# Kernel optimization log

Measured on AMD Instinct MI355X. Metric: run time of the kernel, lower is better.

## Reference

```python
import jax, jax.numpy as jnp
import numpy as np

N, D, K = 8192, 2048, 10000
EPS = 1e-12
COMMITMENT_COST = 0.25


def _l2_normalize(v, axis):
    # matches torch F.normalize(p=2): v / max(||v||, eps)
    n = jnp.linalg.norm(v, axis=axis, keepdims=True)
    return v / jnp.maximum(n, EPS)


def setup_inputs() -> dict:
    key = jax.random.key(0)
    kx, kw = jax.random.split(key)
    x = jax.random.normal(kx, (N, D), dtype=jnp.float32)
    # nn.Embedding weight initialized uniform(0, 3) per the module
    weight = jax.random.uniform(kw, (K, D), dtype=jnp.float32, minval=0.0, maxval=3.0)
    return {"x": x, "weight": weight}


def reference(x, weight):
    # --- get_code_indices ---
    xn = _l2_normalize(x, axis=1)          # [N, D]
    wn = _l2_normalize(weight, axis=1)     # [K, D]
    # ||xn||^2 + ||wn||^2 - 2 xn . wn  -> [N, K]
    distances = (
        jnp.sum(xn * xn, axis=1, keepdims=True)
        + jnp.sum(wn * wn, axis=1)
        - 2.0 * jnp.matmul(xn, wn.T)
    )
    encoding_indices = jnp.argmin(distances, axis=1)  # [N]
    # --- quantize (gathers the UN-normalized codebook, as in the module) ---
    quantized = weight[encoding_indices]              # [N, D]
    # --- training losses ---
    q_latent_loss = jnp.mean((quantized - jax.lax.stop_gradient(x)) ** 2)
    e_latent_loss = jnp.mean((x - jax.lax.stop_gradient(quantized)) ** 2)
    loss = q_latent_loss + COMMITMENT_COST * e_latent_loss
    # straight-through estimator
    quantized = x + jax.lax.stop_gradient(quantized - x)
    return quantized, loss, encoding_indices
```

## Files before the change

### kernel.cpp

```cpp
#include <hip/hip_runtime.h>
#include <math.h>

typedef unsigned short ushort_t;
typedef short short8 __attribute__((ext_vector_type(8)));
typedef float f32x4  __attribute__((ext_vector_type(4)));

#define N_ROWS 8192
#define D_DIM  2048
#define K_CODES 10000
#define EPSF   1e-12f

#define BMT 256
#define BKT 64
#define NT_K 32
#define MTILES 32
#define NTILES 40
#define NGROUP 320

#define BAND_ADD  1e-3f
#define FBIG 1e30f

__device__ __forceinline__ unsigned short f2bf(float f) {
  unsigned u = __float_as_uint(f);
  unsigned r = (u + 0x7fffu + ((u >> 16) & 1u)) >> 16;
  return (unsigned short)r;
}
__device__ __forceinline__ float bf2f(unsigned short h) {
  return __uint_as_float(((unsigned)h) << 16);
}

__device__ __forceinline__ void stage16(const ushort_t* g, ushort_t* l) {
  __builtin_amdgcn_global_load_lds(
      (const __attribute__((address_space(1))) unsigned int*)g,
      (__attribute__((address_space(3))) unsigned int*)l, 16, 0, 0);
}

__device__ __forceinline__ float block_reduce_sum(float v) {
  #pragma unroll
  for (int o = 32; o > 0; o >>= 1) v += __shfl_down(v, o, 64);
  __shared__ float ls[4];
  int lane = threadIdx.x & 63;
  int wid  = threadIdx.x >> 6;
  if (lane == 0) ls[wid] = v;
  __syncthreads();
  v = (threadIdx.x < 4) ? ls[threadIdx.x] : 0.0f;
  if (wid == 0) {
    v += __shfl_down(v, 2, 64);
    v += __shfl_down(v, 1, 64);
  }
  __syncthreads();
  return v;
}

__global__ __launch_bounds__(256) void norm_hi_kernel(
    const float* __restrict__ src, ushort_t* __restrict__ hi,
    float* __restrict__ sq_out, float* __restrict__ inv_out,
    float* __restrict__ hn_out, float* __restrict__ ln_out)
{
  int row = blockIdx.x;
  int tid = threadIdx.x;
  const float* rp = src + (size_t)row * D_DIM;
  float4 v0 = *(const float4*)(rp + tid * 8);
  float4 v1 = *(const float4*)(rp + tid * 8 + 4);
  float s = v0.x*v0.x + v0.y*v0.y + v0.z*v0.z + v0.w*v0.w
          + v1.x*v1.x + v1.y*v1.y + v1.z*v1.z + v1.w*v1.w;
  s = block_reduce_sum(s);
  __shared__ float sh_inv;
  if (tid == 0) sh_inv = 1.0f / fmaxf(sqrtf(s), EPSF);
  __syncthreads();
  float inv = sh_inv;

  float xs[8] = {v0.x, v0.y, v0.z, v0.w, v1.x, v1.y, v1.z, v1.w};
  unsigned short hb[8];
  float t = 0.0f, th = 0.0f, tl = 0.0f;
  #pragma unroll
  for (int i = 0; i < 8; ++i) {
    float xn = xs[i] * inv;
    t += xn * xn;
    unsigned short h = f2bf(xn);
    hb[i] = h;
    float hf = bf2f(h);
    th += hf * hf;
    float l = xn - hf;
    tl += l * l;
  }
  *(short8*)(hi + (size_t)row * D_DIM + tid * 8) = *(short8*)hb;
  t  = block_reduce_sum(t);
  if (tid == 0) sq_out[row] = t;
  th = block_reduce_sum(th);
  if (tid == 0) hn_out[row] = sqrtf(th);
  tl = block_reduce_sum(tl);
  if (tid == 0) { ln_out[row] = sqrtf(tl); inv_out[row] = inv; }
}

__global__ __launch_bounds__(256) void wmax_kernel(
    const float* __restrict__ whn, const float* __restrict__ wln,
    float* __restrict__ wmax_out)
{
  int tid = threadIdx.x;
  float mh = 0.0f, ml = 0.0f;
  for (int k = tid; k < K_CODES; k += 256) {
    mh = fmaxf(mh, whn[k]);
    ml = fmaxf(ml, wln[k]);
  }
  __shared__ float sh[256], sl[256];
  sh[tid] = mh; sl[tid] = ml;
  __syncthreads();
  #pragma unroll
  for (int o = 128; o > 0; o >>= 1) {
    if (tid < o) {
      sh[tid] = fmaxf(sh[tid], sh[tid + o]);
      sl[tid] = fmaxf(sl[tid], sl[tid + o]);
    }
    __syncthreads();
  }
  if (tid == 0) { wmax_out[0] = sh[0]; wmax_out[1] = sl[0]; }
}

#define LEXLT(da, ia, db, ib) ((da) < (db) || ((da) == (db) && (ia) < (ib)))

#define READ_A(mh) { \
  _Pragma("unroll") for (int mi = 0; mi < 4; ++mi) \
  _Pragma("unroll") for (int kc = 0; kc < 2; ++kc) { \
    int r = (mh)*128 + wr*64 + mi*16 + t16; \
    int sl = (kc*4 + h4) ^ (r & 7); \
    af[mi][kc] = *(const short8*)&lA[buf][r*64 + sl*8]; } }

#define READ_B(nh, DST) { \
  _Pragma("unroll") for (int ni = 0; ni < 2; ++ni) \
  _Pragma("unroll") for (int kc = 0; kc < 2; ++kc) { \
    int r = (nh)*128 + wc*32 + ni*16 + t16; \
    int sl = (kc*4 + h4) ^ (r & 7); \
    DST[ni][kc] = *(const short8*)&lB[buf][r*64 + sl*8]; } }

#define MFMA_Q(mh, nh, BF) { \
  _Pragma("unroll") for (int mi = 0; mi < 4; ++mi) \
  _Pragma("unroll") for (int ni = 0; ni < 2; ++ni) \
  _Pragma("unroll") for (int kc = 0; kc < 2; ++kc) \
    acc[(mh)*4+mi][(nh)*2+ni] = __builtin_amdgcn_mfma_f32_16x16x32_bf16( \
        af[mi][kc], BF[ni][kc], acc[(mh)*4+mi][(nh)*2+ni], 0, 0, 0); }

#define STAGE_A(BF, HH, KKO) { \
  stage16(Ah + (size_t)(row0 + (HH)*128 + prow0) * D_DIM + (KKO) + lsl, \
          lA[BF] + (HH)*8192 + c0*512); \
  stage16(Ah + (size_t)(row0 + (HH)*128 + prow1) * D_DIM + (KKO) + lsl, \
          lA[BF] + (HH)*8192 + c0*512 + 512); }

#define STAGE_B(BF, HH, KKO) { \
  int r0_ = col0 + (HH)*128 + prow0; r0_ = r0_ < K_CODES ? r0_ : K_CODES - 1; \
  int r1_ = col0 + (HH)*128 + prow1; r1_ = r1_ < K_CODES ? r1_ : K_CODES - 1; \
  stage16(Bh + (size_t)r0_ * D_DIM + (KKO) + lsl, \
          lB[BF] + (HH)*8192 + c0*512); \
  stage16(Bh + (size_t)r1_ * D_DIM + (KKO) + lsl, \
          lB[BF] + (HH)*8192 + c0*512 + 512); }

__global__ __launch_bounds__(512, 1) void dist_top2_kernel(
    const ushort_t* __restrict__ Ah, const ushort_t* __restrict__ Bh,
    const float* __restrict__ wsq,
    float* __restrict__ p1d, int* __restrict__ p1i, float* __restrict__ p2d)
{
  __shared__ ushort_t lA[2][16384];
  __shared__ ushort_t lB[2][16384];

  const int tid  = threadIdx.x;
  const int lane = tid & 63;
  const int w8   = tid >> 6;
  const int wr   = w8 >> 2;
  const int wc   = w8 & 3;
  const int t16  = lane & 15;
  const int h4   = lane >> 4;

  int bid = blockIdx.x;
  int xcd = bid & 7, l = bid >> 3;
  int ch = l >> 5;
  int wl = l & 31;
  const int mtile = (xcd & 1) * 16 + (wl & 15);
  const int ntile = (xcd >> 1) * 10 + ch * 2 + (wl >> 4);
  const int row0 = mtile * BMT;
  const int col0 = ntile * BMT;

  const int sub  = lane >> 3;
  const int lsl  = ((lane & 7) ^ sub) * 8;
  const int c0   = w8 * 2;
  const int prow0 = c0 * 8 + sub;
  const int prow1 = prow0 + 8;

  f32x4 acc[8][4];
  #pragma unroll
  for (int m = 0; m < 8; ++m)
    #pragma unroll
    for (int n = 0; n < 4; ++n) acc[m][n] = (f32x4){0.f, 0.f, 0.f, 0.f};

  STAGE_A(0, 0, 0);
  STAGE_B(0, 0, 0);
  STAGE_B(0, 1, 0);
  STAGE_A(0, 1, 0);
  asm volatile("s_waitcnt vmcnt(2)" ::: "memory");
  __builtin_amdgcn_s_barrier();

  short8 af[4][2], bfr0[2][2], bfr1[2][2];

  for (int kt = 0; kt < NT_K; ++kt) {
    const int buf  = kt & 1;
    const int nbuf = buf ^ 1;
    const bool hn  = (kt + 1 < NT_K);
    const int kk = (kt + 1) * BKT;

    READ_A(0);
    READ_B(0, bfr0);
    if (hn) STAGE_A(nbuf, 0, kk);
    __builtin_amdgcn_s_barrier();
    asm volatile("s_waitcnt lgkmcnt(0)" ::: "memory");
    __builtin_amdgcn_sched_barrier(0);
    __builtin_amdgcn_s_setprio(1);
    MFMA_Q(0, 0, bfr0);
    __builtin_amdgcn_s_setprio(0);
    __builtin_amdgcn_s_barrier();

    READ_B(1, bfr1);
    if (hn) {
      STAGE_B(nbuf, 0, kk);
      asm volatile("s_waitcnt vmcnt(4)" ::: "memory");
    } else {
      asm volatile("s_waitcnt vmcnt(0)" ::: "memory");
    }
    __builtin_amdgcn_s_barrier();
    asm volatile("s_waitcnt lgkmcnt(0)" ::: "memory");
    __builtin_amdgcn_sched_barrier(0);
    __builtin_amdgcn_s_setprio(1);
    MFMA_Q(0, 1, bfr1);
    __builtin_amdgcn_s_setprio(0);
    __builtin_amdgcn_s_barrier();

    READ_A(1);
    if (hn) STAGE_B(nbuf, 1, kk);
    __builtin_amdgcn_s_barrier();
    asm volatile("s_waitcnt lgkmcnt(0)" ::: "memory");
    __builtin_amdgcn_sched_barrier(0);
    __builtin_amdgcn_s_setprio(1);
    MFMA_Q(1, 1, bfr1);
    __builtin_amdgcn_s_setprio(0);
    __builtin_amdgcn_s_barrier();

    READ_B(0, bfr0);
    if (hn) {
      STAGE_A(nbuf, 1, kk);
      asm volatile("s_waitcnt vmcnt(2)" ::: "memory");
    }
    __builtin_amdgcn_s_barrier();
    asm volatile("s_waitcnt lgkmcnt(0)" ::: "memory");
    __builtin_amdgcn_sched_barrier(0);
    __builtin_amdgcn_s_setprio(1);
    MFMA_Q(1, 0, bfr0);
    __builtin_amdgcn_s_setprio(0);
    __builtin_amdgcn_s_barrier();
  }

  float wsqr[4]; int colr[4];
  #pragma unroll
  for (int n = 0; n < 4; ++n) {
    int col = col0 + ((n & 2) ? 128 : 0) + wc * 32 + ((n & 1) ? 16 : 0) + t16;
    colr[n] = col;
    wsqr[n] = (col < K_CODES) ? wsq[col] : FBIG * 10.0f;
  }
  #pragma unroll
  for (int m = 0; m < 8; ++m) {
    int rloc = ((m & 4) ? 128 : 0) + wr * 64 + (m & 3) * 16 + h4 * 4;
    #pragma unroll
    for (int j = 0; j < 4; ++j) {
      #pragma unroll
      for (int half = 0; half < 2; ++half) {
        int na = half * 2, nb = na + 1;
        float da = wsqr[na] - 2.0f * acc[m][na][j]; int ia = colr[na];
        float db = wsqr[nb] - 2.0f * acc[m][nb][j]; int ib = colr[nb];
        float d1, d2; int i1;
        if (LEXLT(db, ib, da, ia)) { d1 = db; i1 = ib; d2 = da; }
        else                       { d1 = da; i1 = ia; d2 = db; }
        #pragma unroll
        for (int off = 1; off < 16; off <<= 1) {
          float od1 = __shfl_xor(d1, off, 64);
          int   oi1 = __shfl_xor(i1, off, 64);
          float od2 = __shfl_xor(d2, off, 64);
          if (LEXLT(od1, oi1, d1, i1)) { d2 = fminf(d1, od2); d1 = od1; i1 = oi1; }
          else                         { d2 = fminf(od1, d2); }
        }
        if (t16 == 0) {
          int grow = row0 + rloc + j;
          int gid = ntile * 8 + half * 4 + wc;
          size_t o = (size_t)grow * NGROUP + gid;
          p1d[o] = d1; p1i[o] = i1; p2d[o] = d2;
        }
      }
    }
  }
}

__global__ __launch_bounds__(256) void refine_kernel(
    const float* __restrict__ x, const float* __restrict__ w,
    const float* __restrict__ xsq, const float* __restrict__ xinv,
    const float* __restrict__ xhn, const float* __restrict__ xln,
    const float* __restrict__ wsq, const float* __restrict__ winv,
    const float* __restrict__ whn, const float* __restrict__ wln,
    const float* __restrict__ wmax,
    const float* __restrict__ p1d, const int* __restrict__ p1i,
    const float* __restrict__ p2d,
    int* __restrict__ idx_out, float* __restrict__ idxf_out)
{
  const int wv   = threadIdx.x >> 6;
  const int lane = threadIdx.x & 63;
  const int row  = blockIdx.x * 4 + wv;

  const float* xr = x + (size_t)row * D_DIM;
  const float xiv = xinv[row];
  float xv[32];
  #pragma unroll
  for (int j = 0; j < 32; ++j) xv[j] = xr[lane + 64 * j] * xiv;
  const float xs = xsq[row], xh = xhn[row], xl = xln[row];

  const float whm = wmax[0], wlm = wmax[1];
  const float eps_max = 2.0f * (xl * whm + xh * wlm + xl * wlm) + BAND_ADD;

  float gd1[5], gd2[5], geps[5];
  int   gi1[5];
  float tmin = FBIG;
  #pragma unroll
  for (int s = 0; s < 5; ++s) {
    int g = lane + 64 * s;
    size_t o = (size_t)row * NGROUP + g;
    float d1 = p1d[o]; int i1 = p1i[o]; float d2 = p2d[o];
    int is = i1 < K_CODES ? i1 : K_CODES - 1;
    float e1 = 2.0f * (xl * whn[is] + xh * wln[is] + xl * wln[is]) + BAND_ADD;
    gd1[s] = d1; gi1[s] = i1; gd2[s] = d2; geps[s] = e1;
    tmin = fminf(tmin, d1 + e1);
  }
  #pragma unroll
  for (int off = 1; off < 64; off <<= 1) tmin = fminf(tmin, __shfl_xor(tmin, off, 64));
  const float T = tmin;

  float bd = INFINITY; int bi = 0x7fffffff;

  auto refine = [&](int k) {
    const float* wr = w + (size_t)k * D_DIM;
    const float wiv = winv[k];
    float a = 0.0f;
    #pragma unroll
    for (int j = 0; j < 32; ++j) a += xv[j] * (wr[lane + 64 * j] * wiv);
    #pragma unroll
    for (int off = 32; off > 0; off >>= 1) a += __shfl_xor(a, off, 64);
    float df = (xs + wsq[k]) - 2.0f * a;
    if (df < bd || (df == bd && k < bi)) { bd = df; bi = k; }
  };

  #pragma unroll
  for (int s = 0; s < 5; ++s) {
    bool scan = (gd2[s] - eps_max <= T);
    bool cand = !scan && (gd1[s] - geps[s] <= T);
    unsigned long long mcand = __ballot(cand);
    unsigned long long mscan = __ballot(scan);
    while (mcand) {
      int lsrc = __ffsll(mcand) - 1; mcand &= mcand - 1;
      int k = __shfl(gi1[s], lsrc, 64);
      if (k < K_CODES) refine(k);
    }
    while (mscan) {
      int lsrc = __ffsll(mscan) - 1; mscan &= mscan - 1;
      int k0 = (lsrc + 64 * s) * 32;
      for (int kk = 0; kk < 32; ++kk) {
        int k = k0 + kk;
        if (k < K_CODES) refine(k);
      }
    }
  }

  if (lane == 0) { idx_out[row] = bi; idxf_out[row] = (float)bi; }
}

__global__ __launch_bounds__(256) void gather_kernel(
    const float* __restrict__ x, const float* __restrict__ w,
    const int* __restrict__ idx, float* __restrict__ out,
    float* __restrict__ lpart)
{
  int row = blockIdx.x;
  int tid = threadIdx.x;
  int id = idx[row];
  const float4* wr_ = (const float4*)(w + (size_t)id * D_DIM);
  const float4* xr  = (const float4*)(x + (size_t)row * D_DIM);
  float4* outr = (float4*)(out + (size_t)row * D_DIM);
  float s = 0.0f;
  #pragma unroll
  for (int t = 0; t < 2; ++t) {
    int e = tid + t * 256;
    float4 wv = wr_[e], xv = xr[e];
    outr[e] = wv;
    float d0 = wv.x - xv.x, d1 = wv.y - xv.y, d2 = wv.z - xv.z, d3 = wv.w - xv.w;
    s += d0 * d0 + d1 * d1 + d2 * d2 + d3 * d3;
  }
  s = block_reduce_sum(s);
  if (tid == 0) lpart[row] = s;
}

__global__ __launch_bounds__(256) void loss_kernel(const float* __restrict__ lpart,
                                                   float* __restrict__ loss_out)
{
  int tid = threadIdx.x;
  double s = 0.0;
  for (int t = tid; t < N_ROWS; t += 256) s += (double)lpart[t];
  __shared__ double sd[256];
  sd[tid] = s;
  __syncthreads();
  #pragma unroll
  for (int o = 128; o > 0; o >>= 1) {
    if (tid < o) sd[tid] += sd[tid + o];
    __syncthreads();
  }
  if (tid == 0)
    loss_out[0] = (float)(1.25 * sd[0] / (double)((size_t)N_ROWS * (size_t)D_DIM));
}

extern "C" void kernel_launch(void* const* d_in, const int* in_sizes, int n_in,
                              void* d_out, int out_size, void* d_ws, size_t ws_size,
                              hipStream_t stream) {
  const float* x = (const float*)d_in[0];
  const float* w = (const float*)d_in[1];
  float* out = (float*)d_out;
  char*  ws  = (char*)d_ws;

  size_t off = 0;
  auto alloc = [&](size_t bytes) {
    size_t o = off;
    off = (off + bytes + 255) & ~(size_t)255;
    return o;
  };
  const size_t szA1 = (size_t)N_ROWS * D_DIM * 2;
  const size_t szB1 = (size_t)K_CODES * D_DIM * 2;
  const size_t szP  = (size_t)NGROUP * N_ROWS * 4;

  ushort_t* Bh = (ushort_t*)(ws + alloc(szB1));
  float* wsq  = (float*)(ws + alloc((size_t)K_CODES * 4));
  float* winv = (float*)(ws + alloc((size_t)K_CODES * 4));
  float* whn  = (float*)(ws + alloc((size_t)K_CODES * 4));
  float* wln  = (float*)(ws + alloc((size_t)K_CODES * 4));
  float* wmax = (float*)(ws + alloc(2 * 4));
  float* xsq  = (float*)(ws + alloc((size_t)N_ROWS * 4));
  float* xinv = (float*)(ws + alloc((size_t)N_ROWS * 4));
  float* xhn  = (float*)(ws + alloc((size_t)N_ROWS * 4));
  float* xln  = (float*)(ws + alloc((size_t)N_ROWS * 4));
  float* p1d  = (float*)(ws + alloc(szP));
  int*   p1i  = (int*)  (ws + alloc(szP));
  float* p2d  = (float*)(ws + alloc(szP));
  int*   idx  = (int*)  (ws + alloc((size_t)N_ROWS * 4));
  float* lpart = (float*)(ws + alloc((size_t)N_ROWS * 4));

  ushort_t* Ahp;
  if (ws_size >= off + szA1) {
    Ahp = (ushort_t*)(ws + alloc(szA1));
  } else {
    Ahp = (ushort_t*)out;
  }

  float* loss_out = out + (size_t)N_ROWS * D_DIM;
  float* idxf_out = loss_out + 1;

  norm_hi_kernel<<<N_ROWS, 256, 0, stream>>>(x, Ahp, xsq, xinv, xhn, xln);
  norm_hi_kernel<<<K_CODES, 256, 0, stream>>>(w, Bh, wsq, winv, whn, wln);
  wmax_kernel<<<1, 256, 0, stream>>>(whn, wln, wmax);
  dist_top2_kernel<<<MTILES * NTILES, 512, 0, stream>>>(
      Ahp, Bh, wsq, p1d, p1i, p2d);
  refine_kernel<<<N_ROWS / 4, 256, 0, stream>>>(
      x, w, xsq, xinv, xhn, xln, wsq, winv, whn, wln, wmax,
      p1d, p1i, p2d, idx, idxf_out);
  gather_kernel<<<N_ROWS, 256, 0, stream>>>(x, w, idx, out, lpart);
  loss_kernel<<<1, 256, 0, stream>>>(lpart, loss_out);
}
```

Baseline: 901.3 us.

## Tighten refine band, skip unambiguous rows, and relax GEMM pipeline waits

The safety band on the bf16 approximate distances shrinks from 1e-3 to 2e-5. The refine kernel now finds the best approximate candidate first and exits early when it is the only candidate with no group scans. Otherwise it refines that candidate first and uses the exact best distance to prune the remaining candidates and scans, and it loads rows with float4. The GEMM main loop also loosens its vmcnt waits and drops one LDS read/barrier stage to overlap more. The smaller band risks wrong argmin on near-ties, and the removed READ_B may leave bfr0 stale, so correctness is at risk.

```diff
diff --git a/kernel.cpp b/kernel.cpp
--- a/kernel.cpp
+++ b/kernel.cpp
@@ -17,7 +17,7 @@
 #define NTILES 40
 #define NGROUP 320
 
-#define BAND_ADD  1e-3f
+#define BAND_ADD  2e-5f
 #define FBIG 1e30f
 
 __device__ __forceinline__ unsigned short f2bf(float f) {
@@ -195,7 +195,7 @@
   STAGE_B(0, 0, 0);
   STAGE_B(0, 1, 0);
   STAGE_A(0, 1, 0);
-  asm volatile("s_waitcnt vmcnt(2)" ::: "memory");
+  asm volatile("s_waitcnt vmcnt(4)" ::: "memory");
   __builtin_amdgcn_s_barrier();
 
   short8 af[4][2], bfr0[2][2], bfr1[2][2];
@@ -208,7 +208,12 @@
 
     READ_A(0);
     READ_B(0, bfr0);
-    if (hn) STAGE_A(nbuf, 0, kk);
+    if (hn) {
+      STAGE_A(nbuf, 0, kk);
+      asm volatile("s_waitcnt vmcnt(4)" ::: "memory");
+    } else {
+      asm volatile("s_waitcnt vmcnt(2)" ::: "memory");
+    }
     __builtin_amdgcn_s_barrier();
     asm volatile("s_waitcnt lgkmcnt(0)" ::: "memory");
     __builtin_amdgcn_sched_barrier(0);
@@ -242,14 +247,11 @@
     __builtin_amdgcn_s_setprio(0);
     __builtin_amdgcn_s_barrier();
 
-    READ_B(0, bfr0);
     if (hn) {
       STAGE_A(nbuf, 1, kk);
-      asm volatile("s_waitcnt vmcnt(2)" ::: "memory");
-    }
-    __builtin_amdgcn_s_barrier();
-    asm volatile("s_waitcnt lgkmcnt(0)" ::: "memory");
-    __builtin_amdgcn_sched_barrier(0);
+      asm volatile("s_waitcnt vmcnt(4)" ::: "memory");
+    }
+    __builtin_amdgcn_s_barrier();
     __builtin_amdgcn_s_setprio(1);
     MFMA_Q(1, 0, bfr0);
     __builtin_amdgcn_s_setprio(0);
@@ -310,60 +312,95 @@
   const int lane = threadIdx.x & 63;
   const int row  = blockIdx.x * 4 + wv;
 
-  const float* xr = x + (size_t)row * D_DIM;
-  const float xiv = xinv[row];
-  float xv[32];
-  #pragma unroll
-  for (int j = 0; j < 32; ++j) xv[j] = xr[lane + 64 * j] * xiv;
   const float xs = xsq[row], xh = xhn[row], xl = xln[row];
-
   const float whm = wmax[0], wlm = wmax[1];
   const float eps_max = 2.0f * (xl * whm + xh * wlm + xl * wlm) + BAND_ADD;
 
   float gd1[5], gd2[5], geps[5];
   int   gi1[5];
   float tmin = FBIG;
+  float bmind = FBIG, bmine = 0.0f; int bmink = 0x7fffffff;
   #pragma unroll
   for (int s = 0; s < 5; ++s) {
-    int g = lane + 64 * s;
-    size_t o = (size_t)row * NGROUP + g;
+    size_t o = (size_t)row * NGROUP + lane + 64 * s;
     float d1 = p1d[o]; int i1 = p1i[o]; float d2 = p2d[o];
     int is = i1 < K_CODES ? i1 : K_CODES - 1;
     float e1 = 2.0f * (xl * whn[is] + xh * wln[is] + xl * wln[is]) + BAND_ADD;
     gd1[s] = d1; gi1[s] = i1; gd2[s] = d2; geps[s] = e1;
     tmin = fminf(tmin, d1 + e1);
+    if (d1 < bmind || (d1 == bmind && i1 < bmink)) { bmind = d1; bmink = i1; bmine = e1; }
   }
   #pragma unroll
   for (int off = 1; off < 64; off <<= 1) tmin = fminf(tmin, __shfl_xor(tmin, off, 64));
   const float T = tmin;
 
+  #pragma unroll
+  for (int off = 1; off < 64; off <<= 1) {
+    float od = __shfl_xor(bmind, off, 64);
+    int   ok = __shfl_xor(bmink, off, 64);
+    if (od < bmind || (od == bmind && ok < bmink)) { bmind = od; bmink = ok; }
+  }
+  const int kfirst = bmink;
+
+  unsigned long long ms[5], mc[5];
+  int ncand = 0, nscan = 0;
+  #pragma unroll
+  for (int s = 0; s < 5; ++s) {
+    bool scan = (gd2[s] - eps_max <= T);
+    bool cand = !scan && (gd1[s] - geps[s] <= T);
+    ms[s] = __ballot(scan); mc[s] = __ballot(cand);
+    nscan += __popcll(ms[s]); ncand += __popcll(mc[s]);
+  }
+  if (nscan == 0 && ncand == 1) {
+    if (lane == 0) { idx_out[row] = kfirst; idxf_out[row] = (float)kfirst; }
+    return;
+  }
+
+  const float4* xr4 = (const float4*)(x + (size_t)row * D_DIM);
+  const float xiv = xinv[row];
+  float4 xv[8];
+  #pragma unroll
+  for (int j = 0; j < 8; ++j) {
+    float4 v = xr4[lane + 64 * j];
+    v.x *= xiv; v.y *= xiv; v.z *= xiv; v.w *= xiv;
+    xv[j] = v;
+  }
+
   float bd = INFINITY; int bi = 0x7fffffff;
-
   auto refine = [&](int k) {
-    const float* wr = w + (size_t)k * D_DIM;
+    const float4* wr4 = (const float4*)(w + (size_t)k * D_DIM);
     const float wiv = winv[k];
     float a = 0.0f;
     #pragma unroll
-    for (int j = 0; j < 32; ++j) a += xv[j] * (wr[lane + 64 * j] * wiv);
+    for (int j = 0; j < 8; ++j) {
+      float4 wvv = wr4[lane + 64 * j];
+      a += xv[j].x * (wvv.x * wiv) + xv[j].y * (wvv.y * wiv)
+         + xv[j].z * (wvv.z * wiv) + xv[j].w * (wvv.w * wiv);
+    }
     #pragma unroll
     for (int off = 32; off > 0; off >>= 1) a += __shfl_xor(a, off, 64);
     float df = (xs + wsq[k]) - 2.0f * a;
     if (df < bd || (df == bd && k < bi)) { bd = df; bi = k; }
   };
 
+  if (kfirst < K_CODES) refine(kfirst);
+
   #pragma unroll
   for (int s = 0; s < 5; ++s) {
-    bool scan = (gd2[s] - eps_max <= T);
-    bool cand = !scan && (gd1[s] - geps[s] <= T);
-    unsigned long long mcand = __ballot(cand);
-    unsigned long long mscan = __ballot(scan);
-    while (mcand) {
-      int lsrc = __ffsll(mcand) - 1; mcand &= mcand - 1;
+    unsigned long long m = mc[s];
+    while (m) {
+      int lsrc = __ffsll(m) - 1; m &= m - 1;
       int k = __shfl(gi1[s], lsrc, 64);
-      if (k < K_CODES) refine(k);
-    }
-    while (mscan) {
-      int lsrc = __ffsll(mscan) - 1; mscan &= mscan - 1;
+      if (k == kfirst || k >= K_CODES) continue;
+      float a1d = __shfl(gd1[s],  lsrc, 64);
+      float a1e = __shfl(geps[s], lsrc, 64);
+      if (a1d - a1e <= bd + BAND_ADD) refine(k);
+    }
+    m = ms[s];
+    while (m) {
+      int lsrc = __ffsll(m) - 1; m &= m - 1;
+      float a2d = __shfl(gd2[s], lsrc, 64);
+      if (a2d - eps_max > bd + BAND_ADD) continue;
       int k0 = (lsrc + 64 * s) * 32;
       for (int kk = 0; kk < 32; ++kk) {
         int k = k0 + kk;
```

New measurement: 783.5 us. 13.1% less time.
